# Optimization experiments

Measured on AMD Instinct MI355X. Metric: run time of the kernel, lower is better.

Reference implementation:

```python
import jax, jax.numpy as jnp
import numpy as np
import math

NUM_HEAD = 16
HEAD_DIM = 64  # hidden_dim 1024 / 16 heads


def setup_inputs() -> dict:
    key = jax.random.key(0)
    ks = jax.random.split(key, 7)
    N, D = 4096, 1024
    s = 1.0 / math.sqrt(D)
    return {
        "node_emb": jax.random.normal(ks[0], (N, D), jnp.float32),
        "Wq": jax.random.normal(ks[1], (D, D), jnp.float32) * s,
        "bq": jax.random.normal(ks[2], (D,), jnp.float32) * 0.01,
        "Wk": jax.random.normal(ks[3], (D, D), jnp.float32) * s,
        "bk": jax.random.normal(ks[4], (D,), jnp.float32) * 0.01,
        "Wv": jax.random.normal(ks[5], (D, D), jnp.float32) * s,
        "bv": jax.random.normal(ks[6], (D,), jnp.float32) * 0.01,
    }


def reference(node_emb, Wq, bq, Wk, bk, Wv, bv):
    N = node_emb.shape[0]
    # QKV projections (Linear: x @ W^T-style; here W stored [in, out])
    q = (node_emb @ Wq + bq).reshape(N, NUM_HEAD, HEAD_DIM)
    k = (node_emb @ Wk + bk).reshape(N, NUM_HEAD, HEAD_DIM)
    v = (node_emb @ Wv + bv).reshape(N, NUM_HEAD, HEAD_DIM)
    # scores: [h, n_query, n_key]
    scale = 1.0 / math.sqrt(HEAD_DIM)
    scores = jnp.einsum("nhd,mhd->hnm", q, k) * scale
    attn = jax.nn.softmax(scores, axis=-1)
    out = jnp.einsum("hnm,mhd->nhd", attn, v)  # [n, h, d]
    return out.reshape(N, NUM_HEAD * HEAD_DIM)
```

## Files before the change

### kernel.cpp

```cpp
#include <hip/hip_runtime.h>
#include <hip/hip_bf16.h>

#define N_NODES 4096
#define DMODEL  1024
#define NHEAD   16
#define HDIM    64
#define NOUT    3072

typedef __attribute__((ext_vector_type(8))) short short8v;
typedef __attribute__((ext_vector_type(4))) float f32x4;
typedef __attribute__((ext_vector_type(16))) float f32x16;
typedef __attribute__((ext_vector_type(4))) unsigned short ushort4v;
typedef __attribute__((ext_vector_type(4))) unsigned int u32x4;

static __device__ __forceinline__ void gload_lds16(const void* g, void* l) {
  __builtin_amdgcn_global_load_lds((const __attribute__((address_space(1))) void*)g,
                                   (__attribute__((address_space(3))) void*)l, 16, 0, 0);
}

static __device__ __forceinline__ unsigned cvtpk(float a, float b) {
  unsigned r;
  asm("v_cvt_pk_bf16_f32 %0, %1, %2" : "=v"(r) : "v"(a), "v"(b));
  return r;
}

__global__ void cvt_x_kernel(const float* __restrict__ x, __hip_bfloat16* __restrict__ xb) {
  int i = blockIdx.x * blockDim.x + threadIdx.x;
  float4 v = ((const float4*)x)[i];
  union { ushort4v u; __hip_bfloat16 h[4]; } o;
  o.h[0] = __float2bfloat16(v.x);
  o.h[1] = __float2bfloat16(v.y);
  o.h[2] = __float2bfloat16(v.z);
  o.h[3] = __float2bfloat16(v.w);
  ((ushort4v*)xb)[i] = o.u;
}

__global__ void transpose_w_kernel(const float* __restrict__ Wq, const float* __restrict__ Wk,
                                   const float* __restrict__ Wv, __hip_bfloat16* __restrict__ WT) {
  __shared__ float tile[32][33];
  const float* W = blockIdx.z == 0 ? Wq : (blockIdx.z == 1 ? Wk : Wv);
  int o0 = blockIdx.x * 32, i0 = blockIdx.y * 32;
  int tx = threadIdx.x, ty = threadIdx.y;
  {
    float4 v = *(const float4*)&W[(size_t)(i0 + ty) * DMODEL + o0 + tx * 4];
    tile[ty][tx * 4 + 0] = v.x;
    tile[ty][tx * 4 + 1] = v.y;
    tile[ty][tx * 4 + 2] = v.z;
    tile[ty][tx * 4 + 3] = v.w;
  }
  __syncthreads();
  __hip_bfloat16* outp = WT + (size_t)blockIdx.z * DMODEL * DMODEL;
  union { ushort4v u; __hip_bfloat16 h[4]; } o;
#pragma unroll
  for (int c = 0; c < 4; ++c) o.h[c] = __float2bfloat16(tile[tx * 4 + c][ty]);
  *(ushort4v*)&outp[(size_t)(o0 + ty) * DMODEL + i0 + tx * 4] = o.u;
}

__global__ __launch_bounds__(256, 2) void gemm_qkv_kernel(
    const __hip_bfloat16* __restrict__ X, const __hip_bfloat16* __restrict__ WT,
    const float* __restrict__ bq, const float* __restrict__ bk, const float* __restrict__ bv,
    __hip_bfloat16* __restrict__ Qo, __hip_bfloat16* __restrict__ Ko, __hip_bfloat16* __restrict__ Vt) {
  __shared__ __hip_bfloat16 As[128 * 32];
  __shared__ __hip_bfloat16 Bs[128 * 32];
  const int t = threadIdx.x;
  const int lane = t & 63;
  const int w = t >> 6, wr = w >> 1, wc = w & 1;
  const int bm = blockIdx.y, bn = blockIdx.x;

  f32x4 acc[4][4] = {};

  const int rowA = t >> 2;
  const int koff = (t & 3) * 8;
  const __hip_bfloat16* Ag0 = X + (size_t)(bm * 128 + rowA) * DMODEL + koff;
  const __hip_bfloat16* Ag1 = X + (size_t)(bm * 128 + 64 + rowA) * DMODEL + koff;
  const __hip_bfloat16* Bg0 = WT + (size_t)(bn * 128 + rowA) * DMODEL + koff;
  const __hip_bfloat16* Bg1 = WT + (size_t)(bn * 128 + 64 + rowA) * DMODEL + koff;
  __hip_bfloat16* Al0 = &As[t * 8];
  __hip_bfloat16* Al1 = &As[(t + 256) * 8];
  __hip_bfloat16* Bl0 = &Bs[t * 8];
  __hip_bfloat16* Bl1 = &Bs[(t + 256) * 8];

  const short* As_s = (const short*)As;
  const short* Bs_s = (const short*)Bs;
  const int fr = lane & 15, fk = (lane >> 4) * 8;

  for (int kt = 0; kt < DMODEL / 32; ++kt) {
    gload_lds16(Ag0 + kt * 32, Al0);
    gload_lds16(Ag1 + kt * 32, Al1);
    gload_lds16(Bg0 + kt * 32, Bl0);
    gload_lds16(Bg1 + kt * 32, Bl1);
    __syncthreads();
    short8v a[4], b[4];
#pragma unroll
    for (int m = 0; m < 4; ++m)
      a[m] = *(const short8v*)&As_s[(wr * 64 + m * 16 + fr) * 32 + fk];
#pragma unroll
    for (int n = 0; n < 4; ++n)
      b[n] = *(const short8v*)&Bs_s[(wc * 64 + n * 16 + fr) * 32 + fk];
#pragma unroll
    for (int m = 0; m < 4; ++m)
#pragma unroll
      for (int n = 0; n < 4; ++n)
        acc[m][n] = __builtin_amdgcn_mfma_f32_16x16x32_bf16(a[m], b[n], acc[m][n], 0, 0, 0);
    __syncthreads();
  }

  const int row0 = bm * 128 + wr * 64;
  const int col0 = bn * 128 + wc * 64;
  const int which = col0 >> 10;
  const float* bias = which == 0 ? bq : (which == 1 ? bk : bv);
  const float QSCALE = 0.18033688011112042f;
#pragma unroll
  for (int m = 0; m < 4; ++m) {
#pragma unroll
    for (int n = 0; n < 4; ++n) {
#pragma unroll
      for (int i = 0; i < 4; ++i) {
        int r = row0 + m * 16 + (lane >> 4) * 4 + i;
        int c = col0 + n * 16 + (lane & 15);
        int oo = c & 1023;
        float v = acc[m][n][i] + bias[oo];
        if (which == 0) v *= QSCALE;
        int h = oo >> 6, d = oo & 63;
        __hip_bfloat16 hv = __float2bfloat16(v);
        if (which == 0)      Qo[((size_t)h << 18) + r * 64 + d] = hv;
        else if (which == 1) Ko[((size_t)h << 18) + r * 64 + d] = hv;
        else                 Vt[((size_t)h << 18) + d * 4096 + r] = hv;
      }
    }
  }
}

__global__ __launch_bounds__(256, 2) void attn64_kernel(
    const __hip_bfloat16* __restrict__ Q, const __hip_bfloat16* __restrict__ K,
    const __hip_bfloat16* __restrict__ Vt,
    __hip_bfloat16* __restrict__ Opart, float* __restrict__ lpart) {
  __shared__ __align__(16) short lds_k[2][2][64 * 64];
  __shared__ __align__(16) short lds_v[2][2][64 * 64];

  const int bid = blockIdx.x;
  const int lin = (bid & 7) * 64 + (bid >> 3);
  const int h = lin >> 5, qb = (lin & 31) >> 1, split = lin & 1;

  const int t = threadIdx.x, lane = t & 63, w = t >> 6;
  const int lq = lane & 31, hi = lane >> 5;

  const short* Qh = (const short*)Q + ((size_t)h << 18);
  const short* Kh = (const short*)K + ((size_t)h << 18);
  const short* Vh = (const short*)Vt + ((size_t)h << 18);

  const int q0 = qb * 256 + w * 64;

  short8v qfA[4], qfB[4];
#pragma unroll
  for (int kk = 0; kk < 4; ++kk) {
    qfA[kk] = *(const short8v*)&Qh[(q0 + lq) * 64 + kk * 16 + hi * 8];
    qfB[kk] = *(const short8v*)&Qh[(q0 + 32 + lq) * 64 + kk * 16 + hi * 8];
  }

  int off8[2][4];
#pragma unroll
  for (int half = 0; half < 2; ++half)
#pragma unroll
    for (int kk = 0; kk < 4; ++kk)
      off8[half][kk] = (half * 32 + lq) * 64 + (((kk * 2 + hi) ^ (lq & 7)) * 8);

  auto stage = [&](int kt, int p, int s) {
#pragma unroll
    for (int i = 0; i < 2; ++i) {
      int c = w * 128 + i * 64 + lane;
      int row = c >> 3, ss = (c & 7) ^ (row & 7);
      gload_lds16(Kh + (size_t)(kt * 64 + row) * 64 + ss * 8, &lds_k[p][s][c * 8]);
    }
#pragma unroll
    for (int i = 0; i < 2; ++i) {
      int c = w * 128 + i * 64 + lane;
      int row = c >> 3, ss = (c & 7) ^ (row & 7);
      gload_lds16(Vh + (size_t)row * 4096 + kt * 64 + ss * 8, &lds_v[p][s][c * 8]);
    }
  };

  f32x16 oA0 = {}, oA1 = {}, oB0 = {}, oB1 = {};
  float lA_r = 0.f, lB_r = 0.f;

  auto compute = [&](const short* kp, const short* vp) {
    f32x16 sA0 = {}, sA1 = {}, sB0 = {}, sB1 = {};
#pragma unroll
    for (int kk = 0; kk < 4; ++kk) {
      short8v ka0 = *(const short8v*)&kp[off8[0][kk]];
      sA0 = __builtin_amdgcn_mfma_f32_32x32x16_bf16(ka0, qfA[kk], sA0, 0, 0, 0);
      sB0 = __builtin_amdgcn_mfma_f32_32x32x16_bf16(ka0, qfB[kk], sB0, 0, 0, 0);
      short8v ka1 = *(const short8v*)&kp[off8[1][kk]];
      sA1 = __builtin_amdgcn_mfma_f32_32x32x16_bf16(ka1, qfA[kk], sA1, 0, 0, 0);
      sB1 = __builtin_amdgcn_mfma_f32_32x32x16_bf16(ka1, qfB[kk], sB1, 0, 0, 0);
    }
    short8v paA[4], paB[4];
#pragma unroll
    for (int j = 0; j < 16; ++j) { sA0[j] = __builtin_amdgcn_exp2f(sA0[j]); lA_r += sA0[j]; }
#pragma unroll
    for (int j = 0; j < 16; ++j) { sA1[j] = __builtin_amdgcn_exp2f(sA1[j]); lA_r += sA1[j]; }
#pragma unroll
    for (int half = 0; half < 2; ++half) {
      const f32x16& s = half ? sA1 : sA0;
#pragma unroll
      for (int g = 0; g < 2; ++g) {
        unsigned a0 = cvtpk(s[g * 8 + 0], s[g * 8 + 1]), a1 = cvtpk(s[g * 8 + 2], s[g * 8 + 3]);
        unsigned b0 = cvtpk(s[g * 8 + 4], s[g * 8 + 5]), b1 = cvtpk(s[g * 8 + 6], s[g * 8 + 7]);
        asm volatile("v_permlane32_swap_b32 %0, %1" : "+v"(a0), "+v"(b0));
        asm volatile("v_permlane32_swap_b32 %0, %1" : "+v"(a1), "+v"(b1));
        u32x4 u = {a0, a1, b0, b1};
        paA[half * 2 + g] = __builtin_bit_cast(short8v, u);
      }
    }
#pragma unroll
    for (int j = 0; j < 16; ++j) { sB0[j] = __builtin_amdgcn_exp2f(sB0[j]); lB_r += sB0[j]; }
#pragma unroll
    for (int j = 0; j < 16; ++j) { sB1[j] = __builtin_amdgcn_exp2f(sB1[j]); lB_r += sB1[j]; }
#pragma unroll
    for (int half = 0; half < 2; ++half) {
      const f32x16& s = half ? sB1 : sB0;
#pragma unroll
      for (int g = 0; g < 2; ++g) {
        unsigned a0 = cvtpk(s[g * 8 + 0], s[g * 8 + 1]), a1 = cvtpk(s[g * 8 + 2], s[g * 8 + 3]);
        unsigned b0 = cvtpk(s[g * 8 + 4], s[g * 8 + 5]), b1 = cvtpk(s[g * 8 + 6], s[g * 8 + 7]);
        asm volatile("v_permlane32_swap_b32 %0, %1" : "+v"(a0), "+v"(b0));
        asm volatile("v_permlane32_swap_b32 %0, %1" : "+v"(a1), "+v"(b1));
        u32x4 u = {a0, a1, b0, b1};
        paB[half * 2 + g] = __builtin_bit_cast(short8v, u);
      }
    }
#pragma unroll
    for (int kk = 0; kk < 4; ++kk) {
      short8v vb0 = *(const short8v*)&vp[off8[0][kk]];
      oA0 = __builtin_amdgcn_mfma_f32_32x32x16_bf16(paA[kk], vb0, oA0, 0, 0, 0);
      oB0 = __builtin_amdgcn_mfma_f32_32x32x16_bf16(paB[kk], vb0, oB0, 0, 0, 0);
      short8v vb1 = *(const short8v*)&vp[off8[1][kk]];
      oA1 = __builtin_amdgcn_mfma_f32_32x32x16_bf16(paA[kk], vb1, oA1, 0, 0, 0);
      oB1 = __builtin_amdgcn_mfma_f32_32x32x16_bf16(paB[kk], vb1, oB1, 0, 0, 0);
    }
  };

  const int NT = 32;
  const int NIV = NT / 2;
  const int kt0 = split * NT;

  stage(kt0 + 0, 0, 0);
  stage(kt0 + 1, 0, 1);

  for (int iv = 0; iv < NIV; ++iv) {
    const int p = iv & 1;
    __builtin_amdgcn_s_barrier();
    if (iv + 1 < NIV) {
      stage(kt0 + 2 * iv + 2, p ^ 1, 0);
      stage(kt0 + 2 * iv + 3, p ^ 1, 1);
      asm volatile("s_waitcnt vmcnt(8)" ::: "memory");
    } else {
      asm volatile("s_waitcnt vmcnt(0)" ::: "memory");
    }
    __builtin_amdgcn_s_barrier();
    __builtin_amdgcn_sched_barrier(0);
    compute(lds_k[p][0], lds_v[p][0]);
    compute(lds_k[p][1], lds_v[p][1]);
  }

  {
    float lA = lA_r + __shfl_xor(lA_r, 32);
    float lB = lB_r + __shfl_xor(lB_r, 32);
    if (hi == 0) {
      lpart[((split * NHEAD + h) << 12) + q0 + lq] = lA;
      lpart[((split * NHEAD + h) << 12) + q0 + 32 + lq] = lB;
    }
    __hip_bfloat16* Op = Opart + (size_t)split * N_NODES * DMODEL;
#pragma unroll
    for (int r = 0; r < 16; ++r) {
      int ql = (r & 3) + 8 * (r >> 2) + 4 * hi;
      int qgA = q0 + ql, qgB = q0 + 32 + ql;
      Op[(size_t)qgA * DMODEL + (h << 6) + lq] = __float2bfloat16(oA0[r]);
      Op[(size_t)qgA * DMODEL + (h << 6) + 32 + lq] = __float2bfloat16(oA1[r]);
      Op[(size_t)qgB * DMODEL + (h << 6) + lq] = __float2bfloat16(oB0[r]);
      Op[(size_t)qgB * DMODEL + (h << 6) + 32 + lq] = __float2bfloat16(oB1[r]);
    }
  }
}

__global__ void combine_kernel(const __hip_bfloat16* __restrict__ Opart,
                               const float* __restrict__ lpart,
                               float* __restrict__ out) {
  int idx = blockIdx.x * 256 + threadIdx.x;
  int n = idx >> 8;
  int c4 = idx & 255;
  int h = c4 >> 4;
  float l0 = lpart[(h << 12) + n];
  float l1 = lpart[(NHEAD << 12) + (h << 12) + n];
  float inv = 1.0f / (l0 + l1);
  ushort4v a = ((const ushort4v*)Opart)[idx];
  ushort4v b = ((const ushort4v*)(Opart + (size_t)N_NODES * DMODEL))[idx];
  f32x4 o;
#pragma unroll
  for (int j = 0; j < 4; ++j) {
    float fa = __uint_as_float((unsigned)(unsigned short)a[j] << 16);
    float fb = __uint_as_float((unsigned)(unsigned short)b[j] << 16);
    o[j] = (fa + fb) * inv;
  }
  ((f32x4*)out)[idx] = o;
}

__global__ __launch_bounds__(256, 2) void attn_single_kernel(
    const __hip_bfloat16* __restrict__ Q, const __hip_bfloat16* __restrict__ K,
    const __hip_bfloat16* __restrict__ Vt, float* __restrict__ out) {
  __shared__ __align__(16) short lds_k[2][64 * 64];
  __shared__ __align__(16) short lds_v[2][64 * 64];
  __shared__ float smc[4][32];
  const int bid = blockIdx.x;
  const int lin = (bid & 7) * 64 + (bid >> 3);
  const int h = lin >> 5, qb = lin & 31;
  const int t = threadIdx.x, lane = t & 63, w = t >> 6;
  const int lq = lane & 31, hi = lane >> 5;
  const short* Qh = (const short*)Q + ((size_t)h << 18);
  const short* Kh = (const short*)K + ((size_t)h << 18);
  const short* Vh = (const short*)Vt + ((size_t)h << 18);
  const int q0 = qb * 128 + w * 32;
  short8v qf[4];
#pragma unroll
  for (int kk = 0; kk < 4; ++kk)
    qf[kk] = *(const short8v*)&Qh[(q0 + lq) * 64 + kk * 16 + hi * 8];
  int off8[2][4];
#pragma unroll
  for (int half = 0; half < 2; ++half)
#pragma unroll
    for (int kk = 0; kk < 4; ++kk)
      off8[half][kk] = (half * 32 + lq) * 64 + (((kk * 2 + hi) ^ (lq & 7)) * 8);
  auto stage = [&](int kt, int b) {
#pragma unroll
    for (int i = 0; i < 2; ++i) {
      int c = w * 128 + i * 64 + lane;
      int row = c >> 3, ss = (c & 7) ^ (row & 7);
      gload_lds16(Kh + (size_t)(kt * 64 + row) * 64 + ss * 8, &lds_k[b][c * 8]);
    }
#pragma unroll
    for (int i = 0; i < 2; ++i) {
      int c = w * 128 + i * 64 + lane;
      int row = c >> 3, ss = (c & 7) ^ (row & 7);
      gload_lds16(Vh + (size_t)row * 4096 + kt * 64 + ss * 8, &lds_v[b][c * 8]);
    }
  };
  f32x16 o0 = {}, o1 = {};
  float l_r = 0.f;
  stage(0, 0);
  for (int kt = 0; kt < 64; ++kt) {
    const int cur = kt & 1;
    __builtin_amdgcn_s_barrier();
    if (kt + 1 < 64) {
      stage(kt + 1, cur ^ 1);
      asm volatile("s_waitcnt vmcnt(4)" ::: "memory");
    } else {
      asm volatile("s_waitcnt vmcnt(0)" ::: "memory");
    }
    __builtin_amdgcn_s_barrier();
    __builtin_amdgcn_sched_barrier(0);
    const short* kp = lds_k[cur];
    const short* vp = lds_v[cur];
    f32x16 s0 = {}, s1 = {};
#pragma unroll
    for (int kk = 0; kk < 4; ++kk) {
      short8v ka0 = *(const short8v*)&kp[off8[0][kk]];
      s0 = __builtin_amdgcn_mfma_f32_32x32x16_bf16(ka0, qf[kk], s0, 0, 0, 0);
      short8v ka1 = *(const short8v*)&kp[off8[1][kk]];
      s1 = __builtin_amdgcn_mfma_f32_32x32x16_bf16(ka1, qf[kk], s1, 0, 0, 0);
    }
#pragma unroll
    for (int j = 0; j < 16; ++j) { s0[j] = __builtin_amdgcn_exp2f(s0[j]); l_r += s0[j]; }
#pragma unroll
    for (int j = 0; j < 16; ++j) { s1[j] = __builtin_amdgcn_exp2f(s1[j]); l_r += s1[j]; }
    short8v pa[4];
#pragma unroll
    for (int half = 0; half < 2; ++half) {
      const f32x16& s = half ? s1 : s0;
#pragma unroll
      for (int g = 0; g < 2; ++g) {
        unsigned a0 = cvtpk(s[g * 8 + 0], s[g * 8 + 1]), a1 = cvtpk(s[g * 8 + 2], s[g * 8 + 3]);
        unsigned b0 = cvtpk(s[g * 8 + 4], s[g * 8 + 5]), b1 = cvtpk(s[g * 8 + 6], s[g * 8 + 7]);
        asm volatile("v_permlane32_swap_b32 %0, %1" : "+v"(a0), "+v"(b0));
        asm volatile("v_permlane32_swap_b32 %0, %1" : "+v"(a1), "+v"(b1));
        u32x4 u = {a0, a1, b0, b1};
        pa[half * 2 + g] = __builtin_bit_cast(short8v, u);
      }
    }
#pragma unroll
    for (int kk = 0; kk < 4; ++kk) {
      short8v vb0 = *(const short8v*)&vp[off8[0][kk]];
      o0 = __builtin_amdgcn_mfma_f32_32x32x16_bf16(pa[kk], vb0, o0, 0, 0, 0);
      short8v vb1 = *(const short8v*)&vp[off8[1][kk]];
      o1 = __builtin_amdgcn_mfma_f32_32x32x16_bf16(pa[kk], vb1, o1, 0, 0, 0);
    }
  }
  {
    float lt = l_r + __shfl_xor(l_r, 32);
    float inv = 1.0f / lt;
    if (lane < 32) smc[w][lq] = inv;
#pragma unroll
    for (int r = 0; r < 16; ++r) {
      int ql = (r & 3) + 8 * (r >> 2) + 4 * hi;
      float iv = smc[w][ql];
      int qg = q0 + ql;
      out[(size_t)qg * DMODEL + (h << 6) + lq] = o0[r] * iv;
      out[(size_t)qg * DMODEL + (h << 6) + 32 + lq] = o1[r] * iv;
    }
  }
}

extern "C" void kernel_launch(void* const* d_in, const int* in_sizes, int n_in,
                              void* d_out, int out_size, void* d_ws, size_t ws_size,
                              hipStream_t stream) {
  const float* node_emb = (const float*)d_in[0];
  const float* Wq = (const float*)d_in[1];
  const float* bq = (const float*)d_in[2];
  const float* Wk = (const float*)d_in[3];
  const float* bk = (const float*)d_in[4];
  const float* Wv = (const float*)d_in[5];
  const float* bv = (const float*)d_in[6];
  float* out = (float*)d_out;

  const size_t HSZ = (size_t)NHEAD * N_NODES * HDIM;
  __hip_bfloat16* Qb  = (__hip_bfloat16*)d_ws;
  __hip_bfloat16* Kb  = Qb + HSZ;
  __hip_bfloat16* Vtb = Kb + HSZ;
  __hip_bfloat16* Xbf = Vtb + HSZ;
  __hip_bfloat16* WT  = Xbf + (size_t)N_NODES * DMODEL;

  __hip_bfloat16* Opart = Xbf;
  float* lpart = (float*)(Opart + 2 * (size_t)N_NODES * DMODEL);

  const size_t split_bytes =
      (3 * HSZ + 2 * (size_t)N_NODES * DMODEL) * sizeof(__hip_bfloat16) +
      2 * (size_t)NHEAD * N_NODES * sizeof(float);
  const size_t base_bytes =
      (3 * HSZ + (size_t)N_NODES * DMODEL + (size_t)NOUT * DMODEL) * sizeof(__hip_bfloat16);
  const bool can_split = ws_size >= (split_bytes > base_bytes ? split_bytes : base_bytes);

  cvt_x_kernel<<<(N_NODES * DMODEL) / (256 * 4), 256, 0, stream>>>(node_emb, Xbf);
  transpose_w_kernel<<<dim3(32, 32, 3), dim3(8, 32), 0, stream>>>(Wq, Wk, Wv, WT);
  gemm_qkv_kernel<<<dim3(NOUT / 128, N_NODES / 128), 256, 0, stream>>>(
      Xbf, WT, bq, bk, bv, Qb, Kb, Vtb);

  if (can_split) {
    attn64_kernel<<<512, 256, 0, stream>>>(Qb, Kb, Vtb, Opart, lpart);
    combine_kernel<<<(N_NODES * DMODEL) / (256 * 4), 256, 0, stream>>>(Opart, lpart, out);
  } else {
    attn_single_kernel<<<512, 256, 0, stream>>>(Qb, Kb, Vtb, out);
  }
}
```

Before: 134.5 us.

## Fuse input conversion kernels and double-buffer QKV GEMM LDS loads

Merges the X bf16 conversion and the weight transpose into one launch, with branches selected by block index, which removes one kernel launch. The QKV GEMM now keeps two LDS buffers and prefetches the next K tile with direct-to-LDS loads while the current tile's MFMAs run. Explicit vmcnt waits plus raw s_barrier replace the two __syncthreads per iteration. This doubles LDS use per block and depends on hand-placed waitcnt and barrier ordering being correct.

```diff
diff --git a/kernel.cpp b/kernel.cpp
--- a/kernel.cpp
+++ b/kernel.cpp
@@ -24,44 +24,50 @@
   return r;
 }
 
-__global__ void cvt_x_kernel(const float* __restrict__ x, __hip_bfloat16* __restrict__ xb) {
-  int i = blockIdx.x * blockDim.x + threadIdx.x;
-  float4 v = ((const float4*)x)[i];
-  union { ushort4v u; __hip_bfloat16 h[4]; } o;
-  o.h[0] = __float2bfloat16(v.x);
-  o.h[1] = __float2bfloat16(v.y);
-  o.h[2] = __float2bfloat16(v.z);
-  o.h[3] = __float2bfloat16(v.w);
-  ((ushort4v*)xb)[i] = o.u;
-}
-
-__global__ void transpose_w_kernel(const float* __restrict__ Wq, const float* __restrict__ Wk,
-                                   const float* __restrict__ Wv, __hip_bfloat16* __restrict__ WT) {
+__global__ void prep_kernel(const float* __restrict__ x, __hip_bfloat16* __restrict__ xb,
+                            const float* __restrict__ Wq, const float* __restrict__ Wk,
+                            const float* __restrict__ Wv, __hip_bfloat16* __restrict__ WT) {
   __shared__ float tile[32][33];
-  const float* W = blockIdx.z == 0 ? Wq : (blockIdx.z == 1 ? Wk : Wv);
-  int o0 = blockIdx.x * 32, i0 = blockIdx.y * 32;
-  int tx = threadIdx.x, ty = threadIdx.y;
-  {
-    float4 v = *(const float4*)&W[(size_t)(i0 + ty) * DMODEL + o0 + tx * 4];
-    tile[ty][tx * 4 + 0] = v.x;
-    tile[ty][tx * 4 + 1] = v.y;
-    tile[ty][tx * 4 + 2] = v.z;
-    tile[ty][tx * 4 + 3] = v.w;
-  }
-  __syncthreads();
-  __hip_bfloat16* outp = WT + (size_t)blockIdx.z * DMODEL * DMODEL;
-  union { ushort4v u; __hip_bfloat16 h[4]; } o;
-#pragma unroll
-  for (int c = 0; c < 4; ++c) o.h[c] = __float2bfloat16(tile[tx * 4 + c][ty]);
-  *(ushort4v*)&outp[(size_t)(o0 + ty) * DMODEL + i0 + tx * 4] = o.u;
+  const int bid = blockIdx.x;
+  const int t = threadIdx.x;
+  if (bid < 4096) {
+    int i = bid * 256 + t;
+    float4 v = ((const float4*)x)[i];
+    union { ushort4v u; __hip_bfloat16 h[4]; } o;
+    o.h[0] = __float2bfloat16(v.x);
+    o.h[1] = __float2bfloat16(v.y);
+    o.h[2] = __float2bfloat16(v.z);
+    o.h[3] = __float2bfloat16(v.w);
+    ((ushort4v*)xb)[i] = o.u;
+  } else {
+    int b2 = bid - 4096;
+    int z = b2 >> 10, rem = b2 & 1023;
+    int bx = rem & 31, by = rem >> 5;
+    const float* W = z == 0 ? Wq : (z == 1 ? Wk : Wv);
+    int o0 = bx * 32, i0 = by * 32;
+    int tx = t & 7, ty = t >> 3;
+    {
+      float4 v = *(const float4*)&W[(size_t)(i0 + ty) * DMODEL + o0 + tx * 4];
+      tile[ty][tx * 4 + 0] = v.x;
+      tile[ty][tx * 4 + 1] = v.y;
+      tile[ty][tx * 4 + 2] = v.z;
+      tile[ty][tx * 4 + 3] = v.w;
+    }
+    __syncthreads();
+    __hip_bfloat16* outp = WT + (size_t)z * DMODEL * DMODEL;
+    union { ushort4v u; __hip_bfloat16 h[4]; } o;
+#pragma unroll
+    for (int c = 0; c < 4; ++c) o.h[c] = __float2bfloat16(tile[tx * 4 + c][ty]);
+    *(ushort4v*)&outp[(size_t)(o0 + ty) * DMODEL + i0 + tx * 4] = o.u;
+  }
 }
 
 __global__ __launch_bounds__(256, 2) void gemm_qkv_kernel(
     const __hip_bfloat16* __restrict__ X, const __hip_bfloat16* __restrict__ WT,
     const float* __restrict__ bq, const float* __restrict__ bk, const float* __restrict__ bv,
     __hip_bfloat16* __restrict__ Qo, __hip_bfloat16* __restrict__ Ko, __hip_bfloat16* __restrict__ Vt) {
-  __shared__ __hip_bfloat16 As[128 * 32];
-  __shared__ __hip_bfloat16 Bs[128 * 32];
+  __shared__ __hip_bfloat16 As[2][128 * 32];
+  __shared__ __hip_bfloat16 Bs[2][128 * 32];
   const int t = threadIdx.x;
   const int lane = t & 63;
   const int w = t >> 6, wr = w >> 1, wc = w & 1;
@@ -75,21 +81,32 @@
   const __hip_bfloat16* Ag1 = X + (size_t)(bm * 128 + 64 + rowA) * DMODEL + koff;
   const __hip_bfloat16* Bg0 = WT + (size_t)(bn * 128 + rowA) * DMODEL + koff;
   const __hip_bfloat16* Bg1 = WT + (size_t)(bn * 128 + 64 + rowA) * DMODEL + koff;
-  __hip_bfloat16* Al0 = &As[t * 8];
-  __hip_bfloat16* Al1 = &As[(t + 256) * 8];
-  __hip_bfloat16* Bl0 = &Bs[t * 8];
-  __hip_bfloat16* Bl1 = &Bs[(t + 256) * 8];
-
-  const short* As_s = (const short*)As;
-  const short* Bs_s = (const short*)Bs;
+
+  auto stage = [&](int kt, int b) {
+    gload_lds16(Ag0 + kt * 32, &As[b][t * 8]);
+    gload_lds16(Ag1 + kt * 32, &As[b][(t + 256) * 8]);
+    gload_lds16(Bg0 + kt * 32, &Bs[b][t * 8]);
+    gload_lds16(Bg1 + kt * 32, &Bs[b][(t + 256) * 8]);
+  };
+
   const int fr = lane & 15, fk = (lane >> 4) * 8;
 
+  stage(0, 0);
+
   for (int kt = 0; kt < DMODEL / 32; ++kt) {
-    gload_lds16(Ag0 + kt * 32, Al0);
-    gload_lds16(Ag1 + kt * 32, Al1);
-    gload_lds16(Bg0 + kt * 32, Bl0);
-    gload_lds16(Bg1 + kt * 32, Bl1);
-    __syncthreads();
+    const int cur = kt & 1;
+    __builtin_amdgcn_s_barrier();
+    if (kt + 1 < DMODEL / 32) {
+      stage(kt + 1, cur ^ 1);
+      asm volatile("s_waitcnt vmcnt(4)" ::: "memory");
+    } else {
+      asm volatile("s_waitcnt vmcnt(0)" ::: "memory");
+    }
+    __builtin_amdgcn_s_barrier();
+    __builtin_amdgcn_sched_barrier(0);
+
+    const short* As_s = (const short*)As[cur];
+    const short* Bs_s = (const short*)Bs[cur];
     short8v a[4], b[4];
 #pragma unroll
     for (int m = 0; m < 4; ++m)
@@ -102,7 +119,6 @@
 #pragma unroll
       for (int n = 0; n < 4; ++n)
         acc[m][n] = __builtin_amdgcn_mfma_f32_16x16x32_bf16(a[m], b[n], acc[m][n], 0, 0, 0);
-    __syncthreads();
   }
 
   const int row0 = bm * 128 + wr * 64;
@@ -438,8 +454,7 @@
       (3 * HSZ + (size_t)N_NODES * DMODEL + (size_t)NOUT * DMODEL) * sizeof(__hip_bfloat16);
   const bool can_split = ws_size >= (split_bytes > base_bytes ? split_bytes : base_bytes);
 
-  cvt_x_kernel<<<(N_NODES * DMODEL) / (256 * 4), 256, 0, stream>>>(node_emb, Xbf);
-  transpose_w_kernel<<<dim3(32, 32, 3), dim3(8, 32), 0, stream>>>(Wq, Wk, Wv, WT);
+  prep_kernel<<<4096 + 3072, 256, 0, stream>>>(node_emb, Xbf, Wq, Wk, Wv, WT);
   gemm_qkv_kernel<<<dim3(NOUT / 128, N_NODES / 128), 256, 0, stream>>>(
       Xbf, WT, bq, bk, bv, Qb, Kb, Vtb);
 
```

Measured after the change: 131.6 us (median of 2 runs). -2.2%, faster.
